# Optimization experiments

Measured on AMD Instinct MI355X. Metric: run time of the kernel, lower is better.

Reference implementation:

```python
import jax, jax.numpy as jnp
import numpy as np

PAD = 0  # vocab[PADDING]
T, B, S, E, H, V = 32, 32, 200, 512, 512, 50000


def setup_inputs() -> dict:
    key = jax.random.key(0)
    ks = jax.random.split(key, 16)
    u = lambda k, sh, s: jax.random.uniform(k, sh, jnp.float32, -s, s)
    lstm_s = 1.0 / np.sqrt(H)
    inp = {}
    inp["tgt_in"] = jax.random.randint(ks[0], (T, B), 0, V)
    inp["tgt_out"] = jax.random.randint(ks[1], (T, B), 0, V)
    inp["src_lens"] = jax.random.randint(ks[2], (B,), S // 2, S + 1)  # valid lengths >= 1
    inp["src_encodings"] = jax.random.normal(ks[3], (B, S, H), jnp.float32) * 0.1
    inp["last_state"] = jax.random.normal(ks[4], (1, B, H), jnp.float32) * 0.1
    inp["last_cell"] = jax.random.normal(ks[5], (1, B, H), jnp.float32) * 0.1
    inp["embed_table"] = jax.random.normal(ks[6], (V, E), jnp.float32) * 0.02
    in_sz = E + H  # input_feed=True
    inp["W_ih"] = u(ks[7], (4 * H, in_sz), lstm_s)
    inp["W_hh"] = u(ks[8], (4 * H, H), lstm_s)
    inp["b_ih"] = u(ks[9], (4 * H,), lstm_s)
    inp["b_hh"] = u(ks[10], (4 * H,), lstm_s)
    inp["W_attn"] = u(ks[11], (H, 2 * H), 1.0 / np.sqrt(2 * H))  # linear_out, no bias (dot attn)
    inp["W_gen"] = u(ks[12], (H, E + 2 * H), 1.0 / np.sqrt(E + 2 * H))
    inp["b_gen"] = u(ks[13], (H,), 1.0 / np.sqrt(E + 2 * H))
    inp["W_read"] = u(ks[14], (V, H), 1.0 / np.sqrt(H))  # readout, bias=False
    return inp


def reference(tgt_in, tgt_out, src_lens, src_encodings, last_state, last_cell,
              embed_table, W_ih, W_hh, b_ih, b_hh, W_attn, W_gen, b_gen, W_read):
    Bn = tgt_in.shape[1]
    Sn = src_encodings.shape[1]
    Hn = last_state.shape[-1]
    emb = embed_table[tgt_in]  # (T,B,E)
    len_mask = jnp.arange(Sn)[None, :] < src_lens[:, None]  # (B,S)
    h0 = last_state[0]
    c0 = last_cell[0]
    att0 = jnp.zeros((Bn, Hn), emb.dtype)  # att_tm1 init

    def step(carry, y_emb):
        h, c, att = carry
        x = jnp.concatenate([y_emb, att], axis=-1)  # input feed: (B,E+H)
        g = x @ W_ih.T + h @ W_hh.T + b_ih + b_hh  # (B,4H), torch gate order i,f,g,o
        i, f, gg, o = jnp.split(g, 4, axis=-1)
        c_new = jax.nn.sigmoid(f) * c + jax.nn.sigmoid(i) * jnp.tanh(gg)
        h_new = jax.nn.sigmoid(o) * jnp.tanh(c_new)
        # GlobalAttention (dot, softmax), query = last_state
        scores = jnp.einsum('bh,bsh->bs', h_new, src_encodings)  # (B,S)
        scores = jnp.where(len_mask, scores, -jnp.inf)
        alpha = jax.nn.softmax(scores, axis=-1)  # (B,S)
        ctx = jnp.einsum('bs,bsh->bh', alpha, src_encodings)  # (B,H)
        att_t = jnp.tanh(jnp.concatenate([ctx, h_new], axis=-1) @ W_attn.T)  # (B,H)
        cat_final = jnp.concatenate([y_emb, h_new, att_t], axis=-1)  # (B,E+2H)
        dec = jnp.tanh(cat_final @ W_gen.T + b_gen)  # (B,H)
        return (h_new, c_new, att_t), (dec, alpha)

    _, (decs, alphas) = jax.lax.scan(step, (h0, c0, att0), emb)  # decs: (T,B,H)
    logits = decs @ W_read.T  # (T,B,V)
    words_log_prob = jax.nn.log_softmax(logits, axis=-1)
    ys = jnp.argmax(words_log_prob, axis=-1)  # (T,B)
    words_mask = (tgt_out != PAD).astype(words_log_prob.dtype)
    word_losses = -jnp.take_along_axis(words_log_prob, tgt_out[..., None], axis=-1)[..., 0] * words_mask
    return word_losses, ys
```

## Files before the change

### kernel.cpp

```cpp
#include <hip/hip_runtime.h>
#include <math.h>

#define T_ 32
#define B_ 32
#define S_ 200
#define E_ 512
#define H_ 512
#define V_ 50000
#define VP_ 50176
#define G4_ 2048
#define NCH 196

using bf16x8 = __attribute__((ext_vector_type(8))) __bf16;
using f32x4  = __attribute__((ext_vector_type(4))) float;

__device__ __forceinline__ float sigf(float x) { return 1.f / (1.f + expf(-x)); }

__device__ __forceinline__ unsigned short f2bf(float v) {
    unsigned int x = __float_as_uint(v);
    return (unsigned short)((x + 0x7FFFu + ((x >> 16) & 1u)) >> 16);
}
__device__ __forceinline__ float bf2f(unsigned short b) {
    return __uint_as_float(((unsigned int)b) << 16);
}

__device__ __forceinline__ void async16(void* lds, const void* g) {
    __builtin_amdgcn_global_load_lds(
        (const __attribute__((address_space(1))) unsigned int*)g,
        (__attribute__((address_space(3))) unsigned int*)lds, 16, 0, 0);
}

__device__ __forceinline__ void g_store(float* p, float v) {
    __hip_atomic_store(p, v, __ATOMIC_RELAXED, __HIP_MEMORY_SCOPE_AGENT);
}
__device__ __forceinline__ float g_load(const float* p) {
    return __hip_atomic_load(p, __ATOMIC_RELAXED, __HIP_MEMORY_SCOPE_AGENT);
}

__device__ __forceinline__ void full_sync(int* bar, int ep) {
    __syncthreads();
    if (threadIdx.x == 0) {
        const int g = blockIdx.x & 7;
        int a = __hip_atomic_fetch_add(&bar[g * 32], 1, __ATOMIC_RELAXED, __HIP_MEMORY_SCOPE_AGENT);
        if (a == ep * 32 + 31) {
            int q = __hip_atomic_fetch_add(&bar[256], 1, __ATOMIC_RELAXED, __HIP_MEMORY_SCOPE_AGENT);
            if (q == ep * 8 + 7) {
                #pragma unroll
                for (int i = 0; i < 8; i++)
                    __hip_atomic_store(&bar[288 + i * 32], ep + 1, __ATOMIC_RELAXED, __HIP_MEMORY_SCOPE_AGENT);
            }
        }
        while (__hip_atomic_load(&bar[288 + g * 32], __ATOMIC_RELAXED, __HIP_MEMORY_SCOPE_AGENT) < ep + 1)
            __builtin_amdgcn_s_sleep(1);
    }
    __syncthreads();
}

__device__ __forceinline__ void sub_sync(int* bar, int bb, int t) {
    __syncthreads();
    if (threadIdx.x == 0) {
        __hip_atomic_fetch_add(&bar[544 + bb * 32], 1, __ATOMIC_RELAXED, __HIP_MEMORY_SCOPE_AGENT);
        while (__hip_atomic_load(&bar[544 + bb * 32], __ATOMIC_RELAXED, __HIP_MEMORY_SCOPE_AGENT) < (t + 1) * 8)
            __builtin_amdgcn_s_sleep(1);
    }
    __syncthreads();
}

__global__ __launch_bounds__(256) void k_init(const float* __restrict__ last_state,
                                              float* __restrict__ xT) {
    const int f = blockIdx.x * 256 + threadIdx.x;
    xT[f] = 0.f;
    const int k = f >> 5, b = f & 31;
    xT[32768 + f] = last_state[b * 512 + k];
}

__global__ __launch_bounds__(256) void k_g0(const int* __restrict__ tgt_in,
                                            const float* __restrict__ emb,
                                            const float* __restrict__ Wih,
                                            const float* __restrict__ bih,
                                            const float* __restrict__ bhh,
                                            float* __restrict__ G0T) {
    __shared__ float a_s[32][66];
    __shared__ float w_s[32][130];
    const int tid = threadIdx.x;
    const int m0 = blockIdx.x * 64, n0 = blockIdx.y * 128;
    const int mq = tid >> 5, nq = tid & 31;
    float acc[8][4] = {};
    for (int k0 = 0; k0 < 512; k0 += 32) {
        {
            const int mm = tid >> 2, kq = tid & 3, kk = kq * 8;
            const float* row = emb + (size_t)tgt_in[m0 + mm] * E_ + k0 + kk;
            float4 v0 = *(const float4*)(row);
            float4 v1 = *(const float4*)(row + 4);
            a_s[kk + 0][mm] = v0.x; a_s[kk + 1][mm] = v0.y;
            a_s[kk + 2][mm] = v0.z; a_s[kk + 3][mm] = v0.w;
            a_s[kk + 4][mm] = v1.x; a_s[kk + 5][mm] = v1.y;
            a_s[kk + 6][mm] = v1.z; a_s[kk + 7][mm] = v1.w;
        }
        {
            const int nn = tid >> 1, kq = tid & 1, kk = kq * 16;
            const float* row = Wih + (size_t)(n0 + nn) * 1024 + k0 + kk;
            #pragma unroll
            for (int u = 0; u < 4; u++) {
                float4 v = *(const float4*)(row + u * 4);
                w_s[kk + u * 4 + 0][nn] = v.x; w_s[kk + u * 4 + 1][nn] = v.y;
                w_s[kk + u * 4 + 2][nn] = v.z; w_s[kk + u * 4 + 3][nn] = v.w;
            }
        }
        __syncthreads();
        for (int k = 0; k < 32; k++) {
            float a[8], wv[4];
            #pragma unroll
            for (int i = 0; i < 8; i++) a[i] = a_s[k][mq + 8 * i];
            #pragma unroll
            for (int p = 0; p < 4; p++) wv[p] = w_s[k][nq + 32 * p];
            #pragma unroll
            for (int i = 0; i < 8; i++)
                #pragma unroll
                for (int p = 0; p < 4; p++) acc[i][p] += a[i] * wv[p];
        }
        __syncthreads();
    }
    #pragma unroll
    for (int i = 0; i < 8; i++) {
        const int m = m0 + mq + 8 * i;
        #pragma unroll
        for (int p = 0; p < 4; p++) {
            const int n = n0 + nq + 32 * p;
            G0T[(size_t)n * 1024 + m] = acc[i][p] + bih[n] + bhh[n];
        }
    }
}

__global__ __launch_bounds__(256) void k_u(const float* __restrict__ src,
                                           const float* __restrict__ Wattn,
                                           float* __restrict__ U) {
    __shared__ float a_s[32][66];
    __shared__ float w_s[32][130];
    const int tid = threadIdx.x;
    const int m0 = blockIdx.x * 64, n0 = blockIdx.y * 128;
    const int mq = tid >> 5, nq = tid & 31;
    float acc[8][4] = {};
    for (int k0 = 0; k0 < 512; k0 += 32) {
        {
            const int mm = tid >> 2, kq = tid & 3, kk = kq * 8;
            const float* row = src + (size_t)(m0 + mm) * 512 + k0 + kk;
            float4 v0 = *(const float4*)(row);
            float4 v1 = *(const float4*)(row + 4);
            a_s[kk + 0][mm] = v0.x; a_s[kk + 1][mm] = v0.y;
            a_s[kk + 2][mm] = v0.z; a_s[kk + 3][mm] = v0.w;
            a_s[kk + 4][mm] = v1.x; a_s[kk + 5][mm] = v1.y;
            a_s[kk + 6][mm] = v1.z; a_s[kk + 7][mm] = v1.w;
        }
        {
            const int nn = tid >> 1, kq = tid & 1, kk = kq * 16;
            const float* row = Wattn + (size_t)(n0 + nn) * 1024 + k0 + kk;
            #pragma unroll
            for (int u = 0; u < 4; u++) {
                float4 v = *(const float4*)(row + u * 4);
                w_s[kk + u * 4 + 0][nn] = v.x; w_s[kk + u * 4 + 1][nn] = v.y;
                w_s[kk + u * 4 + 2][nn] = v.z; w_s[kk + u * 4 + 3][nn] = v.w;
            }
        }
        __syncthreads();
        for (int k = 0; k < 32; k++) {
            float a[8], wv[4];
            #pragma unroll
            for (int i = 0; i < 8; i++) a[i] = a_s[k][mq + 8 * i];
            #pragma unroll
            for (int p = 0; p < 4; p++) wv[p] = w_s[k][nq + 32 * p];
            #pragma unroll
            for (int i = 0; i < 8; i++)
                #pragma unroll
                for (int p = 0; p < 4; p++) acc[i][p] += a[i] * wv[p];
        }
        __syncthreads();
    }
    #pragma unroll
    for (int i = 0; i < 8; i++) {
        const int m = m0 + mq + 8 * i;
        #pragma unroll
        for (int p = 0; p < 4; p++)
            U[(size_t)m * 512 + n0 + nq + 32 * p] = acc[i][p];
    }
}

__global__ __launch_bounds__(256) void k_tr(const float* __restrict__ Wattn,
                                            float* __restrict__ WaRT) {
    __shared__ float t_s[32][33];
    const int tid = threadIdx.x;
    const int bx = blockIdx.x, by = blockIdx.y;
    {
        const int jj = tid >> 3, kq = (tid & 7) * 4;
        float4 v = *(const float4*)(Wattn + (size_t)(by * 32 + jj) * 1024 + 512 + bx * 32 + kq);
        t_s[jj][kq + 0] = v.x; t_s[jj][kq + 1] = v.y;
        t_s[jj][kq + 2] = v.z; t_s[jj][kq + 3] = v.w;
    }
    __syncthreads();
    {
        const int kk = tid >> 3, jq = (tid & 7) * 4;
        float4 w;
        w.x = t_s[jq + 0][kk]; w.y = t_s[jq + 1][kk];
        w.z = t_s[jq + 2][kk]; w.w = t_s[jq + 3][kk];
        *(float4*)(WaRT + (size_t)(bx * 32 + kk) * 512 + by * 32 + jq) = w;
    }
}

__global__ __launch_bounds__(256) void k_wconv(const float* __restrict__ Wread,
                                               unsigned short* __restrict__ whk,
                                               unsigned short* __restrict__ wlk) {
    const size_t q = (size_t)blockIdx.x * 256 + threadIdx.x;
    const size_t k8 = q * 8;
    const int n = (int)(k8 >> 9);
    const int k = (int)(k8 & 511);
    if (n >= VP_) return;
    uint4 h4, l4;
    if (n < V_) {
        float4 p0 = *(const float4*)(Wread + (size_t)n * 512 + k);
        float4 p1 = *(const float4*)(Wread + (size_t)n * 512 + k + 4);
        float v[8] = {p0.x, p0.y, p0.z, p0.w, p1.x, p1.y, p1.z, p1.w};
        unsigned int hb[8], lb[8];
        #pragma unroll
        for (int e = 0; e < 8; e++) {
            hb[e] = f2bf(v[e]);
            lb[e] = f2bf(v[e] - bf2f((unsigned short)hb[e]));
        }
        h4 = make_uint4(hb[0] | (hb[1] << 16), hb[2] | (hb[3] << 16),
                        hb[4] | (hb[5] << 16), hb[6] | (hb[7] << 16));
        l4 = make_uint4(lb[0] | (lb[1] << 16), lb[2] | (lb[3] << 16),
                        lb[4] | (lb[5] << 16), lb[6] | (lb[7] << 16));
    } else {
        h4 = make_uint4(0, 0, 0, 0);
        l4 = make_uint4(0, 0, 0, 0);
    }
    const int lk = (k >> 3) & 3;
    const size_t dst = (size_t)(k >> 5) * ((size_t)VP_ * 32) + (size_t)n * 32
                     + (size_t)((lk ^ ((n >> 1) & 3)) * 8);
    *(uint4*)(whk + dst) = h4;
    *(uint4*)(wlk + dst) = l4;
}

__global__ __launch_bounds__(512) void k_scan(const float* __restrict__ G0T,
                                              const float* __restrict__ U,
                                              const float* __restrict__ WaRT,
                                              const float* __restrict__ Wih,
                                              const float* __restrict__ Whh,
                                              const float* __restrict__ src,
                                              const int* __restrict__ lens,
                                              const float* __restrict__ last_cell,
                                              float* __restrict__ xT,
                                              float* __restrict__ h_b,
                                              float* __restrict__ scb,
                                              float* __restrict__ h_hist,
                                              float* __restrict__ att_hist,
                                              int* __restrict__ bar) {
    __shared__ float Wl[8 * 1024];
    __shared__ float Ul[200 * 64];
    __shared__ float red_s[2048];
    __shared__ float gate_s[256];
    __shared__ float h_s[512];
    __shared__ float al[256];
    __shared__ float pr[512];

    const int blk = blockIdx.x, tid = threadIdx.x;
    const int u0 = blk * 2;
    const int bb = blk & 31, p = blk >> 5;

    for (int f = tid; f < 2048; f += 512) {
        const int r = f >> 8, k = (f & 255) * 4;
        const int j = (r >> 1) * 512 + u0 + (r & 1);
        float4 v;
        if (k < 512) v = *(const float4*)(Wih + (size_t)j * 1024 + 512 + k);
        else         v = *(const float4*)(Whh + (size_t)j * 512 + (k - 512));
        *(float4*)&Wl[r * 1024 + k] = v;
    }
    for (int f = tid; f < 3200; f += 512) {
        const int s = f >> 4, q = (f & 15) * 4;
        *(float4*)&Ul[s * 64 + q] = *(const float4*)(U + ((size_t)bb * S_ + s) * 512 + p * 64 + q);
    }
    float creg = (tid < 64) ? last_cell[(tid & 31) * 512 + u0 + (tid >> 5)] : 0.f;
    __syncthreads();

    const int w = tid >> 6, lane = tid & 63;
    const int hf = lane >> 5, b = lane & 31;
    const int len = lens[bb];

    for (int t = 0; t < T_; t++) {
        {
            const int hoff = ((t + 1) & 1) * 512;
            const int kbase = w * 128 + hf * 64;
            const float* xp = (kbase < 512)
                ? (xT + (size_t)kbase * 32 + b)
                : (xT + (size_t)(512 + hoff + (kbase - 512)) * 32 + b);
            float acc[8] = {};
            #pragma unroll
            for (int kk = 0; kk < 64; kk += 8) {
                float xv[8];
                #pragma unroll
                for (int i = 0; i < 8; i++)
                    xv[i] = g_load(xp + (size_t)(kk + i) * 32);
                #pragma unroll
                for (int r = 0; r < 8; r++) {
                    const float* wr = &Wl[r * 1024 + kbase + kk];
                    float s0 = xv[0] * wr[0] + xv[1] * wr[1] + xv[2] * wr[2] + xv[3] * wr[3];
                    float s1 = xv[4] * wr[4] + xv[5] * wr[5] + xv[6] * wr[6] + xv[7] * wr[7];
                    acc[r] += s0 + s1;
                }
            }
            #pragma unroll
            for (int r = 0; r < 8; r++) acc[r] += __shfl_xor(acc[r], 32);
            if (hf == 0) {
                #pragma unroll
                for (int r = 0; r < 8; r++) red_s[w * 256 + r * 32 + b] = acc[r];
            }
            __syncthreads();
            if (tid < 256) {
                const int r = tid >> 5, b2 = tid & 31;
                const int j = (r >> 1) * 512 + u0 + (r & 1);
                float g = G0T[(size_t)j * 1024 + t * 32 + b2];
                #pragma unroll
                for (int ww = 0; ww < 8; ww++) g += red_s[ww * 256 + r * 32 + b2];
                gate_s[r * 32 + b2] = g;
            }
            __syncthreads();
            if (tid < 64) {
                const int ui = tid >> 5, b2 = tid & 31, u = u0 + ui;
                const float gi = gate_s[(0 + ui) * 32 + b2];
                const float gf = gate_s[(2 + ui) * 32 + b2];
                const float gg = gate_s[(4 + ui) * 32 + b2];
                const float go = gate_s[(6 + ui) * 32 + b2];
                const float cn = sigf(gf) * creg + sigf(gi) * tanhf(gg);
                const float hn = sigf(go) * tanhf(cn);
                creg = cn;
                g_store(&xT[(size_t)(512 + (t & 1) * 512 + u) * 32 + b2], hn);
                g_store(&h_b[b2 * 512 + u], hn);
                h_hist[((size_t)t * B_ + b2) * 512 + u] = hn;
            }
        }
        full_sync(bar, 2 * t);

        {
            h_s[tid] = g_load(&h_b[bb * 512 + tid]);
            __syncthreads();
            for (int i = w; i < 25; i += 8) {
                const int s = p * 25 + i;
                const float* sr = src + ((size_t)bb * S_ + s) * 512;
                const float4 x0 = *(const float4*)(sr + lane * 4);
                const float4 x1 = *(const float4*)(sr + 256 + lane * 4);
                const float4 h0 = *(const float4*)(&h_s[lane * 4]);
                const float4 h1 = *(const float4*)(&h_s[256 + lane * 4]);
                float a = x0.x * h0.x + x0.y * h0.y + x0.z * h0.z + x0.w * h0.w
                        + x1.x * h1.x + x1.y * h1.y + x1.z * h1.z + x1.w * h1.w;
                #pragma unroll
                for (int mk = 1; mk < 64; mk <<= 1) a += __shfl_xor(a, mk);
                if (lane == 0) g_store(&scb[bb * 256 + s], (s < len) ? a : -INFINITY);
            }
        }
        sub_sync(bar, bb, t);

        {
            if (tid < 64) {
                const float v0 = g_load(&scb[bb * 256 + tid]);
                const float v1 = g_load(&scb[bb * 256 + 64 + tid]);
                const float v2 = g_load(&scb[bb * 256 + 128 + tid]);
                const float v3 = (tid < 8) ? g_load(&scb[bb * 256 + 192 + tid]) : -INFINITY;
                float m = fmaxf(fmaxf(v0, v1), fmaxf(v2, v3));
                #pragma unroll
                for (int mk = 1; mk < 64; mk <<= 1) m = fmaxf(m, __shfl_xor(m, mk));
                const float e0 = expf(v0 - m), e1 = expf(v1 - m), e2 = expf(v2 - m);
                const float e3 = (tid < 8) ? expf(v3 - m) : 0.f;
                float sum = (e0 + e1) + (e2 + e3);
                #pragma unroll
                for (int mk = 1; mk < 64; mk <<= 1) sum += __shfl_xor(sum, mk);
                const float inv = 1.f / sum;
                al[tid] = e0 * inv; al[64 + tid] = e1 * inv; al[128 + tid] = e2 * inv;
                if (tid < 8) al[192 + tid] = e3 * inv;
            }
            __syncthreads();
            const int jl = tid & 63, sg = tid >> 6;
            float uacc = 0.f;
            #pragma unroll 5
            for (int s = sg * 25; s < sg * 25 + 25; s++)
                uacc += al[s] * Ul[s * 64 + jl];
            const float* wc0 = WaRT + (size_t)(sg * 64) * 512 + p * 64 + jl;
            const float* hp = &h_s[sg * 64];
            float c0 = 0.f, c1 = 0.f;
            #pragma unroll 8
            for (int kk = 0; kk < 64; kk += 2) {
                c0 += hp[kk] * wc0[(size_t)kk * 512];
                c1 += hp[kk + 1] * wc0[(size_t)(kk + 1) * 512];
            }
            pr[tid] = uacc + c0 + c1;
            __syncthreads();
            if (tid < 64) {
                float tot = 0.f;
                #pragma unroll
                for (int sgg = 0; sgg < 8; sgg++) tot += pr[sgg * 64 + tid];
                const float a = tanhf(tot);
                g_store(&xT[(size_t)(p * 64 + tid) * 32 + bb], a);
                att_hist[((size_t)t * B_ + bb) * 512 + p * 64 + tid] = a;
            }
        }
        full_sync(bar, 2 * t + 1);
    }
}

__global__ __launch_bounds__(256) void k_dec(const int* __restrict__ tgt_in,
                                             const float* __restrict__ emb,
                                             const float* __restrict__ h_hist,
                                             const float* __restrict__ att_hist,
                                             const float* __restrict__ Wgen,
                                             const float* __restrict__ bgen,
                                             unsigned short* __restrict__ dh,
                                             unsigned short* __restrict__ dl,
                                             unsigned short* __restrict__ dhk,
                                             unsigned short* __restrict__ dlk,
                                             int pre) {
    __shared__ float a_s[32][66];
    __shared__ float w_s[32][130];
    const int tid = threadIdx.x;
    const int m0 = blockIdx.x * 64, n0 = blockIdx.y * 128;
    const int mq = tid >> 5, nq = tid & 31;
    float acc[8][4] = {};
    for (int k0 = 0; k0 < 1536; k0 += 32) {
        {
            const int mm = tid >> 2, kq = tid & 3, kk = kq * 8;
            const int m = m0 + mm;
            const float* row;
            if (k0 < 512)       row = emb + (size_t)tgt_in[m] * E_ + k0;
            else if (k0 < 1024) row = h_hist + (size_t)m * 512 + (k0 - 512);
            else                row = att_hist + (size_t)m * 512 + (k0 - 1024);
            row += kk;
            float4 v0 = *(const float4*)(row);
            float4 v1 = *(const float4*)(row + 4);
            a_s[kk + 0][mm] = v0.x; a_s[kk + 1][mm] = v0.y;
            a_s[kk + 2][mm] = v0.z; a_s[kk + 3][mm] = v0.w;
            a_s[kk + 4][mm] = v1.x; a_s[kk + 5][mm] = v1.y;
            a_s[kk + 6][mm] = v1.z; a_s[kk + 7][mm] = v1.w;
        }
        {
            const int nn = tid >> 1, kq = tid & 1, kk = kq * 16;
            const float* row = Wgen + (size_t)(n0 + nn) * 1536 + k0 + kk;
            #pragma unroll
            for (int u = 0; u < 4; u++) {
                float4 v = *(const float4*)(row + u * 4);
                w_s[kk + u * 4 + 0][nn] = v.x; w_s[kk + u * 4 + 1][nn] = v.y;
                w_s[kk + u * 4 + 2][nn] = v.z; w_s[kk + u * 4 + 3][nn] = v.w;
            }
        }
        __syncthreads();
        for (int k = 0; k < 32; k++) {
            float a[8], wv[4];
            #pragma unroll
            for (int i = 0; i < 8; i++) a[i] = a_s[k][mq + 8 * i];
            #pragma unroll
            for (int pq = 0; pq < 4; pq++) wv[pq] = w_s[k][nq + 32 * pq];
            #pragma unroll
            for (int i = 0; i < 8; i++)
                #pragma unroll
                for (int pq = 0; pq < 4; pq++) acc[i][pq] += a[i] * wv[pq];
        }
        __syncthreads();
    }
    #pragma unroll
    for (int i = 0; i < 8; i++) {
        const int m = m0 + mq + 8 * i;
        #pragma unroll
        for (int pq = 0; pq < 4; pq++) {
            const int n = n0 + nq + 32 * pq;
            const float v = tanhf(acc[i][pq] + bgen[n]);
            const unsigned short hb = f2bf(v);
            const unsigned short lb = f2bf(v - bf2f(hb));
            dh[(size_t)m * 512 + n] = hb;
            dl[(size_t)m * 512 + n] = lb;
            if (pre) {
                const size_t ca = (size_t)(n >> 5) * 32768 + (size_t)(m >> 6) * 2048
                                + (size_t)(m & 63) * 32 + (n & 31);
                dhk[ca] = hb;
                dlk[ca] = lb;
            }
        }
    }
}

__global__ __launch_bounds__(256) void k_read_pre(const unsigned short* __restrict__ dhk,
                                                  const unsigned short* __restrict__ dlk,
                                                  const unsigned short* __restrict__ whk,
                                                  const unsigned short* __restrict__ wlk,
                                                  const int* __restrict__ tgt_out,
                                                  float4* __restrict__ part,
                                                  float* __restrict__ tgt_logit) {
    __shared__ __align__(16) unsigned short BhL[8192];
    __shared__ __align__(16) unsigned short BlL[8192];
    __shared__ float ep_max[64][2];
    __shared__ int   ep_idx[64][2];
    __shared__ float ep_fin[64];
    __shared__ int   ep_fidx[64];
    __shared__ float ep_sum[64][2];

    const int xcd = blockIdx.x & 7;
    const int idx = blockIdx.x >> 3;
    const int mi  = idx & 15;
    const int group = idx >> 4;
    const int ch = group * 8 + xcd;
    if (ch >= NCH) return;
    const int m0 = mi * 64, n0 = ch * 256;

    const int tid = threadIdx.x;
    const int lane = tid & 63, wid = tid >> 6;
    const int wr = wid >> 1, wc = wid & 1;
    const int l15 = lane & 15, lk = lane >> 4;

    f32x4 acc[2][8];
    #pragma unroll
    for (int mt = 0; mt < 2; mt++)
        #pragma unroll
        for (int nt = 0; nt < 8; nt++) acc[mt][nt] = {0.f, 0.f, 0.f, 0.f};

    const unsigned short* bh_src = whk + (size_t)n0 * 32;
    const unsigned short* bl_src = wlk + (size_t)n0 * 32;
    const unsigned short* ah_base = dhk + (size_t)(m0 >> 6) * 2048 + lk * 8;
    const unsigned short* al_base = dlk + (size_t)(m0 >> 6) * 2048 + lk * 8;

    for (int kc = 0; kc < 16; kc++) {
        {
            const size_t cb = (size_t)kc * ((size_t)VP_ * 32);
            const char* gh = (const char*)(bh_src + cb);
            const char* gl = (const char*)(bl_src + cb);
            #pragma unroll
            for (int c = 0; c < 4; c++) {
                const int ob = wid * 4096 + c * 1024;
                async16((char*)BhL + ob, gh + ob + lane * 16);
                async16((char*)BlL + ob, gl + ob + lane * 16);
            }
        }
        bf16x8 afh[2], afl[2];
        {
            const unsigned short* ah = ah_base + (size_t)kc * 32768;
            const unsigned short* al = al_base + (size_t)kc * 32768;
            #pragma unroll
            for (int mt = 0; mt < 2; mt++) {
                const int r = wr * 32 + mt * 16 + l15;
                afh[mt] = *(const bf16x8*)(ah + r * 32);
                afl[mt] = *(const bf16x8*)(al + r * 32);
            }
        }
        __syncthreads();
        #pragma unroll
        for (int nt = 0; nt < 8; nt++) {
            const int nn = wc * 128 + nt * 16 + l15;
            const int bo = nn * 32 + ((lk ^ ((nn >> 1) & 3)) * 8);
            bf16x8 bh = *(const bf16x8*)&BhL[bo];
            bf16x8 bl = *(const bf16x8*)&BlL[bo];
            #pragma unroll
            for (int mt = 0; mt < 2; mt++) {
                acc[mt][nt] = __builtin_amdgcn_mfma_f32_16x16x32_bf16(afh[mt], bh, acc[mt][nt], 0, 0, 0);
                acc[mt][nt] = __builtin_amdgcn_mfma_f32_16x16x32_bf16(afl[mt], bh, acc[mt][nt], 0, 0, 0);
                acc[mt][nt] = __builtin_amdgcn_mfma_f32_16x16x32_bf16(afh[mt], bl, acc[mt][nt], 0, 0, 0);
            }
        }
        __syncthreads();
    }

    #pragma unroll
    for (int mt = 0; mt < 2; mt++)
        #pragma unroll
        for (int reg = 0; reg < 4; reg++) {
            float bv = -INFINITY; int bi = 0x7fffffff;
            #pragma unroll
            for (int nt = 0; nt < 8; nt++) {
                const int n = n0 + wc * 128 + nt * 16 + l15;
                const float v = (n < V_) ? acc[mt][nt][reg] : -INFINITY;
                if (v > bv || (v == bv && n < bi)) { bv = v; bi = n; }
            }
            #pragma unroll
            for (int mk = 1; mk < 16; mk <<= 1) {
                const float ov = __shfl_xor(bv, mk);
                const int oi = __shfl_xor(bi, mk);
                if (ov > bv || (ov == bv && oi < bi)) { bv = ov; bi = oi; }
            }
            if (l15 == 0) {
                const int rl = wr * 32 + mt * 16 + lk * 4 + reg;
                ep_max[rl][wc] = bv; ep_idx[rl][wc] = bi;
            }
        }
    __syncthreads();
    if (tid < 64) {
        const float a = ep_max[tid][0], b = ep_max[tid][1];
        const int ia = ep_idx[tid][0], ib = ep_idx[tid][1];
        const bool tb = (b > a) || (b == a && ib < ia);
        ep_fin[tid] = tb ? b : a; ep_fidx[tid] = tb ? ib : ia;
    }
    __syncthreads();
    #pragma unroll
    for (int mt = 0; mt < 2; mt++)
        #pragma unroll
        for (int reg = 0; reg < 4; reg++) {
            const int rl = wr * 32 + mt * 16 + lk * 4 + reg;
            const float M = ep_fin[rl];
            const int rel = tgt_out[m0 + rl] - n0;
            float se = 0.f;
            #pragma unroll
            for (int nt = 0; nt < 8; nt++) {
                const int nl = wc * 128 + nt * 16 + l15;
                if (n0 + nl < V_) {
                    const float v = acc[mt][nt][reg];
                    se += expf(v - M);
                    if (nl == rel) tgt_logit[m0 + rl] = v;
                }
            }
            #pragma unroll
            for (int mk = 1; mk < 16; mk <<= 1) se += __shfl_xor(se, mk);
            if (l15 == 0) ep_sum[rl][wc] = se;
        }
    __syncthreads();
    if (tid < 64) {
        part[(size_t)(m0 + tid) * NCH + ch] =
            make_float4(ep_fin[tid], ep_sum[tid][0] + ep_sum[tid][1],
                        __int_as_float(ep_fidx[tid]), 0.f);
    }
}

__global__ __launch_bounds__(256) void k_read(const unsigned short* __restrict__ dh,
                                              const unsigned short* __restrict__ dl,
                                              const float* __restrict__ Wread,
                                              const int* __restrict__ tgt_out,
                                              float4* __restrict__ part,
                                              float* __restrict__ tgt_logit) {
    __shared__ __align__(16) unsigned short Bh[4][256][8];
    __shared__ __align__(16) unsigned short Bl[4][256][8];
    __shared__ __align__(16) unsigned short Ah[4][64][8];
    __shared__ __align__(16) unsigned short Alo[4][64][8];
    __shared__ float ep_max[64][2];
    __shared__ int   ep_idx[64][2];
    __shared__ float ep_fin[64];
    __shared__ int   ep_fidx[64];
    __shared__ float ep_sum[64][2];

    const int xcd = blockIdx.x & 7;
    const int idx = blockIdx.x >> 3;
    const int mi  = idx & 15;
    const int group = idx >> 4;
    const int ch = group * 8 + xcd;
    if (ch >= NCH) return;
    const int m0 = mi * 64, n0 = ch * 256;

    const int tid = threadIdx.x;
    const int lane = tid & 63, wid = tid >> 6;
    const int wr = wid >> 1, wc = wid & 1;
    const int l15 = lane & 15, lk = lane >> 4;

    f32x4 acc[2][8];
    #pragma unroll
    for (int mt = 0; mt < 2; mt++)
        #pragma unroll
        for (int nt = 0; nt < 8; nt++) acc[mt][nt] = {0.f, 0.f, 0.f, 0.f};

    for (int kc = 0; kc < 512; kc += 32) {
        {
            const int n = n0 + tid;
            const float* row = Wread + (size_t)n * 512 + kc;
            #pragma unroll
            for (int g = 0; g < 4; g++) {
                uint4 h4, l4;
                if (n < V_) {
                    float4 p0 = *(const float4*)(row + g * 8);
                    float4 p1 = *(const float4*)(row + g * 8 + 4);
                    float v[8] = {p0.x, p0.y, p0.z, p0.w, p1.x, p1.y, p1.z, p1.w};
                    unsigned int hb[8], lb[8];
                    #pragma unroll
                    for (int e = 0; e < 8; e++) {
                        hb[e] = f2bf(v[e]);
                        lb[e] = f2bf(v[e] - bf2f((unsigned short)hb[e]));
                    }
                    h4 = make_uint4(hb[0] | (hb[1] << 16), hb[2] | (hb[3] << 16),
                                    hb[4] | (hb[5] << 16), hb[6] | (hb[7] << 16));
                    l4 = make_uint4(lb[0] | (lb[1] << 16), lb[2] | (lb[3] << 16),
                                    lb[4] | (lb[5] << 16), lb[6] | (lb[7] << 16));
                } else {
                    h4 = make_uint4(0, 0, 0, 0);
                    l4 = make_uint4(0, 0, 0, 0);
                }
                *(uint4*)&Bh[g][tid][0] = h4;
                *(uint4*)&Bl[g][tid][0] = l4;
            }
        }
        {
            const int row = tid >> 2, g = tid & 3;
            *(uint4*)&Ah[g][row][0]  = *(const uint4*)(dh + (size_t)(m0 + row) * 512 + kc + g * 8);
            *(uint4*)&Alo[g][row][0] = *(const uint4*)(dl + (size_t)(m0 + row) * 512 + kc + g * 8);
        }
        __syncthreads();
        {
            bf16x8 afh[2], afl[2];
            #pragma unroll
            for (int mt = 0; mt < 2; mt++) {
                const int r = wr * 32 + mt * 16 + l15;
                afh[mt] = *(const bf16x8*)&Ah[lk][r][0];
                afl[mt] = *(const bf16x8*)&Alo[lk][r][0];
            }
            #pragma unroll
            for (int nt = 0; nt < 8; nt++) {
                const int nn = wc * 128 + nt * 16 + l15;
                bf16x8 bh = *(const bf16x8*)&Bh[lk][nn][0];
                bf16x8 bl = *(const bf16x8*)&Bl[lk][nn][0];
                #pragma unroll
                for (int mt = 0; mt < 2; mt++) {
                    acc[mt][nt] = __builtin_amdgcn_mfma_f32_16x16x32_bf16(afh[mt], bh, acc[mt][nt], 0, 0, 0);
                    acc[mt][nt] = __builtin_amdgcn_mfma_f32_16x16x32_bf16(afl[mt], bh, acc[mt][nt], 0, 0, 0);
                    acc[mt][nt] = __builtin_amdgcn_mfma_f32_16x16x32_bf16(afh[mt], bl, acc[mt][nt], 0, 0, 0);
                }
            }
        }
        __syncthreads();
    }

    #pragma unroll
    for (int mt = 0; mt < 2; mt++)
        #pragma unroll
        for (int reg = 0; reg < 4; reg++) {
            float bv = -INFINITY; int bi = 0x7fffffff;
            #pragma unroll
            for (int nt = 0; nt < 8; nt++) {
                const int n = n0 + wc * 128 + nt * 16 + l15;
                const float v = (n < V_) ? acc[mt][nt][reg] : -INFINITY;
                if (v > bv || (v == bv && n < bi)) { bv = v; bi = n; }
            }
            #pragma unroll
            for (int mk = 1; mk < 16; mk <<= 1) {
                const float ov = __shfl_xor(bv, mk);
                const int oi = __shfl_xor(bi, mk);
                if (ov > bv || (ov == bv && oi < bi)) { bv = ov; bi = oi; }
            }
            if (l15 == 0) {
                const int rl = wr * 32 + mt * 16 + lk * 4 + reg;
                ep_max[rl][wc] = bv; ep_idx[rl][wc] = bi;
            }
        }
    __syncthreads();
    if (tid < 64) {
        const float a = ep_max[tid][0], b = ep_max[tid][1];
        const int ia = ep_idx[tid][0], ib = ep_idx[tid][1];
        const bool tb = (b > a) || (b == a && ib < ia);
        ep_fin[tid] = tb ? b : a; ep_fidx[tid] = tb ? ib : ia;
    }
    __syncthreads();
    #pragma unroll
    for (int mt = 0; mt < 2; mt++)
        #pragma unroll
        for (int reg = 0; reg < 4; reg++) {
            const int rl = wr * 32 + mt * 16 + lk * 4 + reg;
            const float M = ep_fin[rl];
            const int rel = tgt_out[m0 + rl] - n0;
            float se = 0.f;
            #pragma unroll
            for (int nt = 0; nt < 8; nt++) {
                const int nl = wc * 128 + nt * 16 + l15;
                if (n0 + nl < V_) {
                    const float v = acc[mt][nt][reg];
                    se += expf(v - M);
                    if (nl == rel) tgt_logit[m0 + rl] = v;
                }
            }
            #pragma unroll
            for (int mk = 1; mk < 16; mk <<= 1) se += __shfl_xor(se, mk);
            if (l15 == 0) ep_sum[rl][wc] = se;
        }
    __syncthreads();
    if (tid < 64) {
        part[(size_t)(m0 + tid) * NCH + ch] =
            make_float4(ep_fin[tid], ep_sum[tid][0] + ep_sum[tid][1],
                        __int_as_float(ep_fidx[tid]), 0.f);
    }
}

__global__ __launch_bounds__(256) void k_merge(const float4* __restrict__ part,
                                               const float* __restrict__ tgt_logit,
                                               const int* __restrict__ tgt_out,
                                               float* __restrict__ out) {
    const int tid = threadIdx.x;
    const int w = tid >> 6, lane = tid & 63;
    const int row = blockIdx.x * 4 + w;
    float bm = -INFINITY; int bi = 0x7fffffff;
    for (int ch = lane; ch < NCH; ch += 64) {
        const float4 p = part[(size_t)row * NCH + ch];
        const int pi = __float_as_int(p.z);
        if (p.x > bm || (p.x == bm && pi < bi)) { bm = p.x; bi = pi; }
    }
    #pragma unroll
    for (int mk = 1; mk < 64; mk <<= 1) {
        const float ov = __shfl_xor(bm, mk);
        const int oi = __shfl_xor(bi, mk);
        if (ov > bm || (ov == bm && oi < bi)) { bm = ov; bi = oi; }
    }
    float sum = 0.f;
    for (int ch = lane; ch < NCH; ch += 64) {
        const float4 p = part[(size_t)row * NCH + ch];
        sum += p.y * expf(p.x - bm);
    }
    #pragma unroll
    for (int mk = 1; mk < 64; mk <<= 1) sum += __shfl_xor(sum, mk);
    if (lane == 0) {
        const float lse = bm + logf(sum);
        const int tg = tgt_out[row];
        const float loss = (tg != 0) ? (lse - tgt_logit[row]) : 0.f;
        out[row] = loss;
        out[1024 + row] = (float)bi;
    }
}

extern "C" void kernel_launch(void* const* d_in, const int* in_sizes, int n_in,
                              void* d_out, int out_size, void* d_ws, size_t ws_size,
                              hipStream_t stream) {
    const int* tgt_in = (const int*)d_in[0];
    const int* tgt_out = (const int*)d_in[1];
    const int* src_lens = (const int*)d_in[2];
    const float* src = (const float*)d_in[3];
    const float* last_state = (const float*)d_in[4];
    const float* last_cell = (const float*)d_in[5];
    const float* emb = (const float*)d_in[6];
    const float* Wih = (const float*)d_in[7];
    const float* Whh = (const float*)d_in[8];
    const float* bih = (const float*)d_in[9];
    const float* bhh = (const float*)d_in[10];
    const float* Wattn = (const float*)d_in[11];
    const float* Wgen = (const float*)d_in[12];
    const float* bgen = (const float*)d_in[13];
    const float* Wread = (const float*)d_in[14];
    float* out = (float*)d_out;

    float* ws = (float*)d_ws;
    float* G0T      = ws;
    float* U        = G0T + 2097152;
    float* WaRT     = U + 3276800;
    unsigned short* dh  = (unsigned short*)(WaRT + 262144);
    unsigned short* dl  = dh + 524288;
    unsigned short* dhk = dl + 524288;
    unsigned short* dlk = dhk + 524288;
    float* h_hist   = (float*)(dlk + 524288);
    float* att_hist = h_hist + 524288;
    float* xT       = att_hist + 524288;
    float* h_b      = xT + 49152;
    float* scb      = h_b + 16384;
    float4* part    = (float4*)(scb + 8192);
    float* tgtl     = ((float*)part) + 802816;
    int* bar        = (int*)(tgtl + 1024);
    unsigned short* whk = (unsigned short*)(bar + 2048);
    unsigned short* wlk = whk + (size_t)VP_ * 512;

    const size_t need = (size_t)((char*)(wlk + (size_t)VP_ * 512) - (char*)ws);
    const int pre = (ws_size >= need) ? 1 : 0;

    hipMemsetAsync(bar, 0, 8192, stream);

    k_init<<<64, 256, 0, stream>>>(last_state, xT);
    k_g0<<<dim3(16, 16), 256, 0, stream>>>(tgt_in, emb, Wih, bih, bhh, G0T);
    k_u<<<dim3(100, 4), 256, 0, stream>>>(src, Wattn, U);
    k_tr<<<dim3(16, 16), 256, 0, stream>>>(Wattn, WaRT);
    if (pre)
        k_wconv<<<12544, 256, 0, stream>>>(Wread, whk, wlk);

    k_scan<<<256, 512, 0, stream>>>(G0T, U, WaRT, Wih, Whh, src, src_lens, last_cell,
                                    xT, h_b, scb, h_hist, att_hist, bar);

    k_dec<<<dim3(16, 4), 256, 0, stream>>>(tgt_in, emb, h_hist, att_hist, Wgen, bgen,
                                           dh, dl, dhk, dlk, pre);
    if (pre)
        k_read_pre<<<3200, 256, 0, stream>>>(dhk, dlk, whk, wlk, tgt_out, part, tgtl);
    else
        k_read<<<3200, 256, 0, stream>>>(dh, dl, Wread, tgt_out, part, tgtl);
    k_merge<<<256, 256, 0, stream>>>(part, tgtl, tgt_out, out);
}
```

Baseline: 1.025 ms.

## Compute attention scores per block redundantly and double-buffer readout LDS tiles

In the recurrent scan kernel, each block now computes all source-position scores for its batch row into shared memory instead of splitting them across 8 blocks and exchanging through global memory with a per-batch barrier. This removes one cross-block synchronization and a global round-trip per timestep, at the cost of redundant source reads per block. The readout GEMM kernel double-buffers its shared-memory weight tiles so the next chunk's async loads overlap the current chunk's MFMAs, which doubles LDS use.

Result: slower. 1.258 ms (+22.8%).

```diff
diff --git a/kernel.cpp b/kernel.cpp
--- a/kernel.cpp
+++ b/kernel.cpp
@@ -51,16 +51,6 @@
             }
         }
         while (__hip_atomic_load(&bar[288 + g * 32], __ATOMIC_RELAXED, __HIP_MEMORY_SCOPE_AGENT) < ep + 1)
-            __builtin_amdgcn_s_sleep(1);
-    }
-    __syncthreads();
-}
-
-__device__ __forceinline__ void sub_sync(int* bar, int bb, int t) {
-    __syncthreads();
-    if (threadIdx.x == 0) {
-        __hip_atomic_fetch_add(&bar[544 + bb * 32], 1, __ATOMIC_RELAXED, __HIP_MEMORY_SCOPE_AGENT);
-        while (__hip_atomic_load(&bar[544 + bb * 32], __ATOMIC_RELAXED, __HIP_MEMORY_SCOPE_AGENT) < (t + 1) * 8)
             __builtin_amdgcn_s_sleep(1);
     }
     __syncthreads();
@@ -250,7 +240,6 @@
                                               const float* __restrict__ last_cell,
                                               float* __restrict__ xT,
                                               float* __restrict__ h_b,
-                                              float* __restrict__ scb,
                                               float* __restrict__ h_hist,
                                               float* __restrict__ att_hist,
                                               int* __restrict__ bar) {
@@ -259,6 +248,7 @@
     __shared__ float red_s[2048];
     __shared__ float gate_s[256];
     __shared__ float h_s[512];
+    __shared__ float sc_s[200];
     __shared__ float al[256];
     __shared__ float pr[512];
 
@@ -342,8 +332,7 @@
         {
             h_s[tid] = g_load(&h_b[bb * 512 + tid]);
             __syncthreads();
-            for (int i = w; i < 25; i += 8) {
-                const int s = p * 25 + i;
+            for (int s = w; s < S_; s += 8) {
                 const float* sr = src + ((size_t)bb * S_ + s) * 512;
                 const float4 x0 = *(const float4*)(sr + lane * 4);
                 const float4 x1 = *(const float4*)(sr + 256 + lane * 4);
@@ -353,17 +342,14 @@
                         + x1.x * h1.x + x1.y * h1.y + x1.z * h1.z + x1.w * h1.w;
                 #pragma unroll
                 for (int mk = 1; mk < 64; mk <<= 1) a += __shfl_xor(a, mk);
-                if (lane == 0) g_store(&scb[bb * 256 + s], (s < len) ? a : -INFINITY);
-            }
-        }
-        sub_sync(bar, bb, t);
-
-        {
+                if (lane == 0) sc_s[s] = (s < len) ? a : -INFINITY;
+            }
+            __syncthreads();
             if (tid < 64) {
-                const float v0 = g_load(&scb[bb * 256 + tid]);
-                const float v1 = g_load(&scb[bb * 256 + 64 + tid]);
-                const float v2 = g_load(&scb[bb * 256 + 128 + tid]);
-                const float v3 = (tid < 8) ? g_load(&scb[bb * 256 + 192 + tid]) : -INFINITY;
+                const float v0 = sc_s[tid];
+                const float v1 = sc_s[64 + tid];
+                const float v2 = sc_s[128 + tid];
+                const float v3 = (tid < 8) ? sc_s[192 + tid] : -INFINITY;
                 float m = fmaxf(fmaxf(v0, v1), fmaxf(v2, v3));
                 #pragma unroll
                 for (int mk = 1; mk < 64; mk <<= 1) m = fmaxf(m, __shfl_xor(m, mk));
@@ -490,8 +476,8 @@
                                                   const int* __restrict__ tgt_out,
                                                   float4* __restrict__ part,
                                                   float* __restrict__ tgt_logit) {
-    __shared__ __align__(16) unsigned short BhL[8192];
-    __shared__ __align__(16) unsigned short BlL[8192];
+    __shared__ __align__(16) unsigned short BhL[2][8192];
+    __shared__ __align__(16) unsigned short BlL[2][8192];
     __shared__ float ep_max[64][2];
     __shared__ int   ep_idx[64][2];
     __shared__ float ep_fin[64];
@@ -522,18 +508,20 @@
     const unsigned short* ah_base = dhk + (size_t)(m0 >> 6) * 2048 + lk * 8;
     const unsigned short* al_base = dlk + (size_t)(m0 >> 6) * 2048 + lk * 8;
 
+    {
+        const char* gh = (const char*)bh_src;
+        const char* gl = (const char*)bl_src;
+        #pragma unroll
+        for (int c = 0; c < 4; c++) {
+            const int ob = wid * 4096 + c * 1024;
+            async16((char*)&BhL[0][0] + ob, gh + ob + lane * 16);
+            async16((char*)&BlL[0][0] + ob, gl + ob + lane * 16);
+        }
+    }
+    __syncthreads();
+
     for (int kc = 0; kc < 16; kc++) {
-        {
-            const size_t cb = (size_t)kc * ((size_t)VP_ * 32);
-            const char* gh = (const char*)(bh_src + cb);
-            const char* gl = (const char*)(bl_src + cb);
-            #pragma unroll
-            for (int c = 0; c < 4; c++) {
-                const int ob = wid * 4096 + c * 1024;
-                async16((char*)BhL + ob, gh + ob + lane * 16);
-                async16((char*)BlL + ob, gl + ob + lane * 16);
-            }
-        }
+        const int cur = kc & 1;
         bf16x8 afh[2], afl[2];
         {
             const unsigned short* ah = ah_base + (size_t)kc * 32768;
@@ -545,13 +533,23 @@
                 afl[mt] = *(const bf16x8*)(al + r * 32);
             }
         }
-        __syncthreads();
+        if (kc < 15) {
+            const size_t cb = (size_t)(kc + 1) * ((size_t)VP_ * 32);
+            const char* gh = (const char*)(bh_src + cb);
+            const char* gl = (const char*)(bl_src + cb);
+            #pragma unroll
+            for (int c = 0; c < 4; c++) {
+                const int ob = wid * 4096 + c * 1024;
+                async16((char*)&BhL[cur ^ 1][0] + ob, gh + ob + lane * 16);
+                async16((char*)&BlL[cur ^ 1][0] + ob, gl + ob + lane * 16);
+            }
+        }
         #pragma unroll
         for (int nt = 0; nt < 8; nt++) {
             const int nn = wc * 128 + nt * 16 + l15;
             const int bo = nn * 32 + ((lk ^ ((nn >> 1) & 3)) * 8);
-            bf16x8 bh = *(const bf16x8*)&BhL[bo];
-            bf16x8 bl = *(const bf16x8*)&BlL[bo];
+            bf16x8 bh = *(const bf16x8*)&BhL[cur][bo];
+            bf16x8 bl = *(const bf16x8*)&BlL[cur][bo];
             #pragma unroll
             for (int mt = 0; mt < 2; mt++) {
                 acc[mt][nt] = __builtin_amdgcn_mfma_f32_16x16x32_bf16(afh[mt], bh, acc[mt][nt], 0, 0, 0);
@@ -861,7 +859,7 @@
         k_wconv<<<12544, 256, 0, stream>>>(Wread, whk, wlk);
 
     k_scan<<<256, 512, 0, stream>>>(G0T, U, WaRT, Wih, Whh, src, src_lens, last_cell,
-                                    xT, h_b, scb, h_hist, att_hist, bar);
+                                    xT, h_b, h_hist, att_hist, bar);
 
     k_dec<<<dim3(16, 4), 256, 0, stream>>>(tgt_in, emb, h_hist, att_hist, Wgen, bgen,
                                            dh, dl, dhk, dlk, pre);
```

## Double-buffer readout B tiles and widen M tile to 128 rows

Applied to the files above, without the earlier changes.

The precomputed-layout readout GEMM now uses two LDS buffers for the W_read tiles. The next K chunk is prefetched asynchronously while MFMAs run on the current one, which removes one barrier per iteration. Each block also covers 128 rows instead of 64, so every loaded W_read tile feeds twice as many MFMAs and the grid halves to 1600 blocks. The cost is doubled accumulator registers and LDS, which may lower occupancy, and fewer blocks in flight.

Measured after the change: 1.182 ms. +15.3%, slower.

```diff
diff --git a/kernel.cpp b/kernel.cpp
--- a/kernel.cpp
+++ b/kernel.cpp
@@ -490,102 +490,122 @@
                                                   const int* __restrict__ tgt_out,
                                                   float4* __restrict__ part,
                                                   float* __restrict__ tgt_logit) {
-    __shared__ __align__(16) unsigned short BhL[8192];
-    __shared__ __align__(16) unsigned short BlL[8192];
-    __shared__ float ep_max[64][2];
-    __shared__ int   ep_idx[64][2];
-    __shared__ float ep_fin[64];
-    __shared__ int   ep_fidx[64];
-    __shared__ float ep_sum[64][2];
+    __shared__ __align__(16) unsigned short BhL[2][8192];
+    __shared__ __align__(16) unsigned short BlL[2][8192];
+    __shared__ float ep_max[128][2];
+    __shared__ int   ep_idx[128][2];
+    __shared__ float ep_fin[128];
+    __shared__ int   ep_fidx[128];
+    __shared__ float ep_sum[128][2];
 
     const int xcd = blockIdx.x & 7;
     const int idx = blockIdx.x >> 3;
-    const int mi  = idx & 15;
-    const int group = idx >> 4;
+    const int m2  = idx & 7;
+    const int group = idx >> 3;
     const int ch = group * 8 + xcd;
     if (ch >= NCH) return;
-    const int m0 = mi * 64, n0 = ch * 256;
+    const int m0 = m2 * 128, n0 = ch * 256;
 
     const int tid = threadIdx.x;
     const int lane = tid & 63, wid = tid >> 6;
     const int wr = wid >> 1, wc = wid & 1;
     const int l15 = lane & 15, lk = lane >> 4;
 
-    f32x4 acc[2][8];
-    #pragma unroll
-    for (int mt = 0; mt < 2; mt++)
-        #pragma unroll
-        for (int nt = 0; nt < 8; nt++) acc[mt][nt] = {0.f, 0.f, 0.f, 0.f};
+    f32x4 acc[2][2][8];
+    #pragma unroll
+    for (int mh = 0; mh < 2; mh++)
+        #pragma unroll
+        for (int mt = 0; mt < 2; mt++)
+            #pragma unroll
+            for (int nt = 0; nt < 8; nt++) acc[mh][mt][nt] = {0.f, 0.f, 0.f, 0.f};
 
     const unsigned short* bh_src = whk + (size_t)n0 * 32;
     const unsigned short* bl_src = wlk + (size_t)n0 * 32;
     const unsigned short* ah_base = dhk + (size_t)(m0 >> 6) * 2048 + lk * 8;
     const unsigned short* al_base = dlk + (size_t)(m0 >> 6) * 2048 + lk * 8;
 
+    {
+        const char* gh = (const char*)bh_src;
+        const char* gl = (const char*)bl_src;
+        #pragma unroll
+        for (int c = 0; c < 4; c++) {
+            const int ob = wid * 4096 + c * 1024;
+            async16((char*)&BhL[0][0] + ob, gh + ob + lane * 16);
+            async16((char*)&BlL[0][0] + ob, gl + ob + lane * 16);
+        }
+    }
+    __syncthreads();
+
     for (int kc = 0; kc < 16; kc++) {
-        {
-            const size_t cb = (size_t)kc * ((size_t)VP_ * 32);
+        const int cur = kc & 1;
+        bf16x8 afh[2][2], afl[2][2];
+        {
+            const unsigned short* ah = ah_base + (size_t)kc * 32768;
+            const unsigned short* al = al_base + (size_t)kc * 32768;
+            #pragma unroll
+            for (int mh = 0; mh < 2; mh++)
+                #pragma unroll
+                for (int mt = 0; mt < 2; mt++) {
+                    const int r = wr * 32 + mt * 16 + l15;
+                    afh[mh][mt] = *(const bf16x8*)(ah + mh * 2048 + r * 32);
+                    afl[mh][mt] = *(const bf16x8*)(al + mh * 2048 + r * 32);
+                }
+        }
+        if (kc < 15) {
+            const size_t cb = (size_t)(kc + 1) * ((size_t)VP_ * 32);
             const char* gh = (const char*)(bh_src + cb);
             const char* gl = (const char*)(bl_src + cb);
             #pragma unroll
             for (int c = 0; c < 4; c++) {
                 const int ob = wid * 4096 + c * 1024;
-                async16((char*)BhL + ob, gh + ob + lane * 16);
-                async16((char*)BlL + ob, gl + ob + lane * 16);
-            }
-        }
-        bf16x8 afh[2], afl[2];
-        {
-            const unsigned short* ah = ah_base + (size_t)kc * 32768;
-            const unsigned short* al = al_base + (size_t)kc * 32768;
-            #pragma unroll
-            for (int mt = 0; mt < 2; mt++) {
-                const int r = wr * 32 + mt * 16 + l15;
-                afh[mt] = *(const bf16x8*)(ah + r * 32);
-                afl[mt] = *(const bf16x8*)(al + r * 32);
-            }
-        }
-        __syncthreads();
+                async16((char*)&BhL[cur ^ 1][0] + ob, gh + ob + lane * 16);
+                async16((char*)&BlL[cur ^ 1][0] + ob, gl + ob + lane * 16);
+            }
+        }
         #pragma unroll
         for (int nt = 0; nt < 8; nt++) {
             const int nn = wc * 128 + nt * 16 + l15;
             const int bo = nn * 32 + ((lk ^ ((nn >> 1) & 3)) * 8);
-            bf16x8 bh = *(const bf16x8*)&BhL[bo];
-            bf16x8 bl = *(const bf16x8*)&BlL[bo];
-            #pragma unroll
-            for (int mt = 0; mt < 2; mt++) {
-                acc[mt][nt] = __builtin_amdgcn_mfma_f32_16x16x32_bf16(afh[mt], bh, acc[mt][nt], 0, 0, 0);
-                acc[mt][nt] = __builtin_amdgcn_mfma_f32_16x16x32_bf16(afl[mt], bh, acc[mt][nt], 0, 0, 0);
-                acc[mt][nt] = __builtin_amdgcn_mfma_f32_16x16x32_bf16(afh[mt], bl, acc[mt][nt], 0, 0, 0);
-            }
+            bf16x8 bh = *(const bf16x8*)&BhL[cur][bo];
+            bf16x8 bl = *(const bf16x8*)&BlL[cur][bo];
+            #pragma unroll
+            for (int mh = 0; mh < 2; mh++)
+                #pragma unroll
+                for (int mt = 0; mt < 2; mt++) {
+                    acc[mh][mt][nt] = __builtin_amdgcn_mfma_f32_16x16x32_bf16(afh[mh][mt], bh, acc[mh][mt][nt], 0, 0, 0);
+                    acc[mh][mt][nt] = __builtin_amdgcn_mfma_f32_16x16x32_bf16(afl[mh][mt], bh, acc[mh][mt][nt], 0, 0, 0);
+                    acc[mh][mt][nt] = __builtin_amdgcn_mfma_f32_16x16x32_bf16(afh[mh][mt], bl, acc[mh][mt][nt], 0, 0, 0);
+                }
         }
         __syncthreads();
     }
 
     #pragma unroll
-    for (int mt = 0; mt < 2; mt++)
-        #pragma unroll
-        for (int reg = 0; reg < 4; reg++) {
-            float bv = -INFINITY; int bi = 0x7fffffff;
-            #pragma unroll
-            for (int nt = 0; nt < 8; nt++) {
-                const int n = n0 + wc * 128 + nt * 16 + l15;
-                const float v = (n < V_) ? acc[mt][nt][reg] : -INFINITY;
-                if (v > bv || (v == bv && n < bi)) { bv = v; bi = n; }
-            }
-            #pragma unroll
-            for (int mk = 1; mk < 16; mk <<= 1) {
-                const float ov = __shfl_xor(bv, mk);
-                const int oi = __shfl_xor(bi, mk);
-                if (ov > bv || (ov == bv && oi < bi)) { bv = ov; bi = oi; }
-            }
-            if (l15 == 0) {
-                const int rl = wr * 32 + mt * 16 + lk * 4 + reg;
-                ep_max[rl][wc] = bv; ep_idx[rl][wc] = bi;
-            }
-        }
-    __syncthreads();
-    if (tid < 64) {
+    for (int mh = 0; mh < 2; mh++)
+        #pragma unroll
+        for (int mt = 0; mt < 2; mt++)
+            #pragma unroll
+            for (int reg = 0; reg < 4; reg++) {
+                float bv = -INFINITY; int bi = 0x7fffffff;
+                #pragma unroll
+                for (int nt = 0; nt < 8; nt++) {
+                    const int n = n0 + wc * 128 + nt * 16 + l15;
+                    const float v = (n < V_) ? acc[mh][mt][nt][reg] : -INFINITY;
+                    if (v > bv || (v == bv && n < bi)) { bv = v; bi = n; }
+                }
+                #pragma unroll
+                for (int mk = 1; mk < 16; mk <<= 1) {
+                    const float ov = __shfl_xor(bv, mk);
+                    const int oi = __shfl_xor(bi, mk);
+                    if (ov > bv || (ov == bv && oi < bi)) { bv = ov; bi = oi; }
+                }
+                if (l15 == 0) {
+                    const int rl = mh * 64 + wr * 32 + mt * 16 + lk * 4 + reg;
+                    ep_max[rl][wc] = bv; ep_idx[rl][wc] = bi;
+                }
+            }
+    __syncthreads();
+    if (tid < 128) {
         const float a = ep_max[tid][0], b = ep_max[tid][1];
         const int ia = ep_idx[tid][0], ib = ep_idx[tid][1];
         const bool tb = (b > a) || (b == a && ib < ia);
@@ -593,28 +613,30 @@
     }
     __syncthreads();
     #pragma unroll
-    for (int mt = 0; mt < 2; mt++)
-        #pragma unroll
-        for (int reg = 0; reg < 4; reg++) {
-            const int rl = wr * 32 + mt * 16 + lk * 4 + reg;
-            const float M = ep_fin[rl];
-            const int rel = tgt_out[m0 + rl] - n0;
-            float se = 0.f;
-            #pragma unroll
-            for (int nt = 0; nt < 8; nt++) {
-                const int nl = wc * 128 + nt * 16 + l15;
-                if (n0 + nl < V_) {
-                    const float v = acc[mt][nt][reg];
-                    se += expf(v - M);
-                    if (nl == rel) tgt_logit[m0 + rl] = v;
-                }
-            }
-            #pragma unroll
-            for (int mk = 1; mk < 16; mk <<= 1) se += __shfl_xor(se, mk);
-            if (l15 == 0) ep_sum[rl][wc] = se;
-        }
-    __syncthreads();
-    if (tid < 64) {
+    for (int mh = 0; mh < 2; mh++)
+        #pragma unroll
+        for (int mt = 0; mt < 2; mt++)
+            #pragma unroll
+            for (int reg = 0; reg < 4; reg++) {
+                const int rl = mh * 64 + wr * 32 + mt * 16 + lk * 4 + reg;
+                const float M = ep_fin[rl];
+                const int rel = tgt_out[m0 + rl] - n0;
+                float se = 0.f;
+                #pragma unroll
+                for (int nt = 0; nt < 8; nt++) {
+                    const int nl = wc * 128 + nt * 16 + l15;
+                    if (n0 + nl < V_) {
+                        const float v = acc[mh][mt][nt][reg];
+                        se += expf(v - M);
+                        if (nl == rel) tgt_logit[m0 + rl] = v;
+                    }
+                }
+                #pragma unroll
+                for (int mk = 1; mk < 16; mk <<= 1) se += __shfl_xor(se, mk);
+                if (l15 == 0) ep_sum[rl][wc] = se;
+            }
+    __syncthreads();
+    if (tid < 128) {
         part[(size_t)(m0 + tid) * NCH + ch] =
             make_float4(ep_fin[tid], ep_sum[tid][0] + ep_sum[tid][1],
                         __int_as_float(ep_fidx[tid]), 0.f);
@@ -866,7 +888,7 @@
     k_dec<<<dim3(16, 4), 256, 0, stream>>>(tgt_in, emb, h_hist, att_hist, Wgen, bgen,
                                            dh, dl, dhk, dlk, pre);
     if (pre)
-        k_read_pre<<<3200, 256, 0, stream>>>(dhk, dlk, whk, wlk, tgt_out, part, tgtl);
+        k_read_pre<<<1600, 256, 0, stream>>>(dhk, dlk, whk, wlk, tgt_out, part, tgtl);
     else
         k_read<<<3200, 256, 0, stream>>>(dh, dl, Wread, tgt_out, part, tgtl);
     k_merge<<<256, 256, 0, stream>>>(part, tgtl, tgt_out, out);
```

## Replace fp32 prologue GEMMs with split-bf16 MFMA kernels

Applied to the files above, without the earlier changes.

Adds a conversion kernel that splits the source encodings, the attention weight half, the W_ih input half and the gathered embeddings into high/low bf16 pairs. A new MFMA GEMM kernel then computes U and G0T with three bf16 products per tile, standing in for the scalar fp32 k_u and k_g0 kernels. This moves the precompute GEMMs onto matrix cores while keeping near-fp32 accuracy. It costs extra workspace and an added conversion pass, and the GEMM loads operands straight from global memory with no LDS staging.

Measured after the change: 1.022 ms. Within noise of the previous version (-0.3%).

```diff
diff --git a/kernel.cpp b/kernel.cpp
--- a/kernel.cpp
+++ b/kernel.cpp
@@ -72,6 +72,118 @@
     xT[f] = 0.f;
     const int k = f >> 5, b = f & 31;
     xT[32768 + f] = last_state[b * 512 + k];
+}
+
+#define CVT_R0 819200
+#define CVT_R1 (CVT_R0 + 65536)
+#define CVT_R2 (CVT_R1 + 262144)
+#define CVT_R3 (CVT_R2 + 131072)
+__global__ __launch_bounds__(256) void k_cvt(const float* __restrict__ src,
+                                             const float* __restrict__ Wattn,
+                                             const float* __restrict__ Wih,
+                                             const float* __restrict__ emb,
+                                             const int* __restrict__ tgt_in,
+                                             unsigned short* __restrict__ sh,
+                                             unsigned short* __restrict__ sl,
+                                             unsigned short* __restrict__ wah,
+                                             unsigned short* __restrict__ wal,
+                                             unsigned short* __restrict__ wih_h,
+                                             unsigned short* __restrict__ wih_l,
+                                             unsigned short* __restrict__ eh,
+                                             unsigned short* __restrict__ el) {
+    const int u = blockIdx.x * 256 + threadIdx.x;
+    if (u >= CVT_R3) return;
+    const float* sp;
+    unsigned short *dh_, *dl_;
+    size_t doff;
+    if (u < CVT_R0) {
+        sp = src + (size_t)u * 4;
+        dh_ = sh; dl_ = sl; doff = (size_t)u * 4;
+    } else if (u < CVT_R1) {
+        const int idx = u - CVT_R0;
+        const int k4 = idx & 127, n = idx >> 7;
+        sp = Wattn + (size_t)n * 1024 + k4 * 4;
+        dh_ = wah; dl_ = wal; doff = (size_t)n * 512 + k4 * 4;
+    } else if (u < CVT_R2) {
+        const int idx = u - CVT_R1;
+        const int k4 = idx & 127, j = idx >> 7;
+        sp = Wih + (size_t)j * 1024 + k4 * 4;
+        dh_ = wih_h; dl_ = wih_l; doff = (size_t)j * 512 + k4 * 4;
+    } else {
+        const int idx = u - CVT_R2;
+        const int k4 = idx & 127, m = idx >> 7;
+        sp = emb + (size_t)tgt_in[m] * 512 + k4 * 4;
+        dh_ = eh; dl_ = el; doff = (size_t)m * 512 + k4 * 4;
+    }
+    const float4 v = *(const float4*)sp;
+    const float vv[4] = {v.x, v.y, v.z, v.w};
+    unsigned int hb[4], lb[4];
+    #pragma unroll
+    for (int e = 0; e < 4; e++) {
+        hb[e] = f2bf(vv[e]);
+        lb[e] = f2bf(vv[e] - bf2f((unsigned short)hb[e]));
+    }
+    *(uint2*)(dh_ + doff) = make_uint2(hb[0] | (hb[1] << 16), hb[2] | (hb[3] << 16));
+    *(uint2*)(dl_ + doff) = make_uint2(lb[0] | (lb[1] << 16), lb[2] | (lb[3] << 16));
+}
+
+__global__ __launch_bounds__(256) void k_gbt(const unsigned short* __restrict__ Ah,
+                                             const unsigned short* __restrict__ Al,
+                                             const unsigned short* __restrict__ Bh,
+                                             const unsigned short* __restrict__ Bl,
+                                             const float* __restrict__ bih,
+                                             const float* __restrict__ bhh,
+                                             float* __restrict__ out,
+                                             int nbn, int mode) {
+    const int m0 = (blockIdx.x / nbn) * 64;
+    const int n0 = (blockIdx.x % nbn) * 256;
+    const int tid = threadIdx.x;
+    const int lane = tid & 63, wid = tid >> 6;
+    const int wr = wid >> 1, wc = wid & 1;
+    const int l15 = lane & 15, lk = lane >> 4;
+
+    f32x4 acc[2][8];
+    #pragma unroll
+    for (int mt = 0; mt < 2; mt++)
+        #pragma unroll
+        for (int nt = 0; nt < 8; nt++) acc[mt][nt] = {0.f, 0.f, 0.f, 0.f};
+
+    for (int kc = 0; kc < 512; kc += 32) {
+        bf16x8 afh[2], afl[2];
+        #pragma unroll
+        for (int mt = 0; mt < 2; mt++) {
+            const int r = wr * 32 + mt * 16 + l15;
+            const size_t ao = (size_t)(m0 + r) * 512 + kc + lk * 8;
+            afh[mt] = *(const bf16x8*)(Ah + ao);
+            afl[mt] = *(const bf16x8*)(Al + ao);
+        }
+        #pragma unroll
+        for (int nt = 0; nt < 8; nt++) {
+            const int nn = wc * 128 + nt * 16 + l15;
+            const size_t bo = (size_t)(n0 + nn) * 512 + kc + lk * 8;
+            bf16x8 bh = *(const bf16x8*)(Bh + bo);
+            bf16x8 bl = *(const bf16x8*)(Bl + bo);
+            #pragma unroll
+            for (int mt = 0; mt < 2; mt++) {
+                acc[mt][nt] = __builtin_amdgcn_mfma_f32_16x16x32_bf16(afh[mt], bh, acc[mt][nt], 0, 0, 0);
+                acc[mt][nt] = __builtin_amdgcn_mfma_f32_16x16x32_bf16(afl[mt], bh, acc[mt][nt], 0, 0, 0);
+                acc[mt][nt] = __builtin_amdgcn_mfma_f32_16x16x32_bf16(afh[mt], bl, acc[mt][nt], 0, 0, 0);
+            }
+        }
+    }
+    #pragma unroll
+    for (int mt = 0; mt < 2; mt++)
+        #pragma unroll
+        for (int reg = 0; reg < 4; reg++) {
+            const int row = m0 + wr * 32 + mt * 16 + lk * 4 + reg;
+            #pragma unroll
+            for (int nt = 0; nt < 8; nt++) {
+                const int col = n0 + wc * 128 + nt * 16 + l15;
+                const float v = acc[mt][nt][reg];
+                if (mode == 0) out[(size_t)row * 512 + col] = v;
+                else           out[(size_t)col * 1024 + row] = v + bih[col] + bhh[col];
+            }
+        }
 }
 
 __global__ __launch_bounds__(256) void k_g0(const int* __restrict__ tgt_in,
@@ -847,15 +959,30 @@
     int* bar        = (int*)(tgtl + 1024);
     unsigned short* whk = (unsigned short*)(bar + 2048);
     unsigned short* wlk = whk + (size_t)VP_ * 512;
-
-    const size_t need = (size_t)((char*)(wlk + (size_t)VP_ * 512) - (char*)ws);
+    unsigned short* sh    = wlk + (size_t)VP_ * 512;
+    unsigned short* sl    = sh + 3276800;
+    unsigned short* wah   = sl + 3276800;
+    unsigned short* wal   = wah + 262144;
+    unsigned short* wih_h = wal + 262144;
+    unsigned short* wih_l = wih_h + 1048576;
+    unsigned short* eh    = wih_l + 1048576;
+    unsigned short* el    = eh + 524288;
+
+    const size_t need = (size_t)((char*)(el + 524288) - (char*)ws);
     const int pre = (ws_size >= need) ? 1 : 0;
 
     hipMemsetAsync(bar, 0, 8192, stream);
 
     k_init<<<64, 256, 0, stream>>>(last_state, xT);
-    k_g0<<<dim3(16, 16), 256, 0, stream>>>(tgt_in, emb, Wih, bih, bhh, G0T);
-    k_u<<<dim3(100, 4), 256, 0, stream>>>(src, Wattn, U);
+    if (pre) {
+        k_cvt<<<(CVT_R3 + 255) / 256, 256, 0, stream>>>(src, Wattn, Wih, emb, tgt_in,
+                                                        sh, sl, wah, wal, wih_h, wih_l, eh, el);
+        k_gbt<<<200, 256, 0, stream>>>(sh, sl, wah, wal, nullptr, nullptr, U, 2, 0);
+        k_gbt<<<128, 256, 0, stream>>>(eh, el, wih_h, wih_l, bih, bhh, G0T, 8, 1);
+    } else {
+        k_g0<<<dim3(16, 16), 256, 0, stream>>>(tgt_in, emb, Wih, bih, bhh, G0T);
+        k_u<<<dim3(100, 4), 256, 0, stream>>>(src, Wattn, U);
+    }
     k_tr<<<dim3(16, 16), 256, 0, stream>>>(Wattn, WaRT);
     if (pre)
         k_wconv<<<12544, 256, 0, stream>>>(Wread, whk, wlk);
```
